# Kernel tuning notes

Measured on AMD Instinct MI355X. Metric: run time of the kernel, lower is better.

Reference implementation:

```python
import jax, jax.numpy as jnp
import numpy as np

B, T, L, V, E, H = 128, 64, 2, 32000, 768, 768
G = 4 * H  # gate dim
EPS = 1e-5


def setup_inputs() -> dict:
    key = jax.random.key(0)
    ks = jax.random.split(key, 12)
    s = 1.0 / np.sqrt(H)
    message = jax.random.randint(ks[0], (B, T), 0, V, dtype=jnp.int64)
    message_lengths = jax.random.randint(ks[1], (B,), 1, T + 1, dtype=jnp.int64)
    return {
        "message": message,
        "message_lengths": message_lengths,
        "embedding_table": jax.random.normal(ks[2], (V, E), jnp.float32),
        "W_ih": jax.random.uniform(ks[3], (L, G, E), jnp.float32, -s, s),
        "W_hh": jax.random.uniform(ks[4], (L, G, H), jnp.float32, -s, s),
        "b_ih": jax.random.uniform(ks[5], (L, G), jnp.float32, -s, s),
        "b_hh": jax.random.uniform(ks[6], (L, G), jnp.float32, -s, s),
        "gamma_h": 1.0 + 0.1 * jax.random.normal(ks[7], (H,), jnp.float32),
        "beta_h": 0.1 * jax.random.normal(ks[8], (H,), jnp.float32),
        "gamma_c": 1.0 + 0.1 * jax.random.normal(ks[9], (H,), jnp.float32),
        "beta_c": 0.1 * jax.random.normal(ks[10], (H,), jnp.float32),
    }


def _layernorm(x, g, b):
    mu = jnp.mean(x, axis=-1, keepdims=True)
    var = jnp.mean(jnp.square(x - mu), axis=-1, keepdims=True)
    return (x - mu) * jax.lax.rsqrt(var + EPS) * g + b


def reference(message, message_lengths, embedding_table, W_ih, W_hh, b_ih, b_hh,
              gamma_h, beta_h, gamma_c, beta_c):
    emb = embedding_table[message]  # [B, T, E]
    # Precompute input projections for all steps/layers (every layer sees the
    # raw embedding at each step, matching the original code).
    x_proj = jnp.einsum('bte,lge->tblg', emb, W_ih) + b_ih  # [T, B, L, G]
    mask = jnp.ones((B, H), emb.dtype)  # dropout_rate=None -> ones mask

    h0 = jnp.zeros((L, B, H), emb.dtype)
    c0 = jnp.zeros((L, B, H), emb.dtype)

    def step(carry, x_t):  # x_t: [B, L, G]
        h, c = carry
        new_h, new_c = [], []
        h_last = None
        for l in range(L):
            gates = x_t[:, l] + h[l] @ W_hh[l].T + b_hh[l]  # [B, G]
            i_g, f_g, g_g, o_g = jnp.split(gates, 4, axis=-1)
            c_t = jax.nn.sigmoid(f_g) * c[l] + jax.nn.sigmoid(i_g) * jnp.tanh(g_g)
            h_t = jax.nn.sigmoid(o_g) * jnp.tanh(c_t)
            h_t = _layernorm(h_t * mask, gamma_h, beta_h)
            c_t = _layernorm(c_t, gamma_c, beta_c)
            new_h.append(h_t)
            new_c.append(c_t)
            h_last = h_t
        return (jnp.stack(new_h), jnp.stack(new_c)), h_last

    _, hidden_all = jax.lax.scan(step, (h0, c0), x_proj)  # [T, B, H]
    hidden_all = hidden_all.transpose(1, 0, 2)  # [B, T, H]
    idx = (message_lengths - 1)[:, None, None]  # [B, 1, 1]
    encoded = jnp.take_along_axis(hidden_all, idx, axis=1)[:, 0]  # [B, H]
    return encoded
```

## Files before the change

### kernel.cpp

```cpp
#include <hip/hip_runtime.h>
#include <stdint.h>

#define T_LEN 64
#define B_SZ  128
#define H_SZ  768
#define G_SZ  3072
#define E_SZ  768
#define LN_EPS 1e-5f

typedef __bf16 bf16x8 __attribute__((ext_vector_type(8)));
typedef float  f32x4  __attribute__((ext_vector_type(4)));
typedef short  short8 __attribute__((ext_vector_type(8)));

__device__ __forceinline__ float bf2f(unsigned short h) {
  unsigned int u = ((unsigned int)h) << 16;
  return __builtin_bit_cast(float, u);
}
__device__ __forceinline__ unsigned short f2bf(float f) {
  unsigned int u = __builtin_bit_cast(unsigned int, f);
  u += 0x7fffu + ((u >> 16) & 1u);
  return (unsigned short)(u >> 16);
}
__device__ __forceinline__ void split8(float4 v0, float4 v1, short8& hi, short8& lo) {
  float v[8] = {v0.x, v0.y, v0.z, v0.w, v1.x, v1.y, v1.z, v1.w};
#pragma unroll
  for (int j = 0; j < 8; ++j) {
    unsigned short h = f2bf(v[j]);
    hi[j] = (short)h;
    lo[j] = (short)f2bf(v[j] - bf2f(h));
  }
}
__device__ __forceinline__ void st_wt(void* p, unsigned long long v) {
  __hip_atomic_store((unsigned long long*)p, v, __ATOMIC_RELAXED,
                     __HIP_MEMORY_SCOPE_AGENT);
}

__global__ void prep_kernel(const int* __restrict__ msg,
                            const float* __restrict__ table,
                            const float* __restrict__ W_ih,
                            const float* __restrict__ W_hh,
                            const float* __restrict__ b_ih,
                            const float* __restrict__ b_hh,
                            const float* __restrict__ gamma_h,
                            const float* __restrict__ beta_h,
                            unsigned short* __restrict__ A_hi,
                            unsigned short* __restrict__ A_lo,
                            unsigned short* __restrict__ Wih_hi,
                            unsigned short* __restrict__ Wih_lo,
                            unsigned short* __restrict__ Whh_hi,
                            unsigned short* __restrict__ Whh_lo,
                            float* __restrict__ SWp,
                            float* __restrict__ Sbeta,
                            float* __restrict__ bias,
                            unsigned int* __restrict__ bar) {
  int idx = blockIdx.x * blockDim.x + threadIdx.x;
  int stride = gridDim.x * blockDim.x;
  for (int c = idx; c < 8192 * 96; c += stride) {
    int n = c / 96;
    int ko = (c - n * 96) * 8;
    int b = n & 127, t = n >> 7;
    int m = msg[b * T_LEN + t];
    const float4* s4 = (const float4*)(table + (size_t)m * E_SZ + ko);
    short8 hi, lo;
    split8(s4[0], s4[1], hi, lo);
    *(short8*)(A_hi + (size_t)n * E_SZ + ko) = hi;
    *(short8*)(A_lo + (size_t)n * E_SZ + ko) = lo;
  }
  for (int c = idx; c < G_SZ * E_SZ / 8; c += stride) {
    int o8 = c * 8;
    {
      const float4* s4 = (const float4*)(W_ih + (size_t)G_SZ * E_SZ + o8);
      short8 hi, lo;
      split8(s4[0], s4[1], hi, lo);
      *(short8*)(Wih_hi + o8) = hi;
      *(short8*)(Wih_lo + o8) = lo;
    }
    {
      int g = o8 / H_SZ;
      int j = o8 - g * H_SZ;
      const float4* s4 = (const float4*)(W_hh + (size_t)G_SZ * H_SZ + o8);
      const float4* g4 = (const float4*)(gamma_h + j);
      float4 v0 = s4[0], v1 = s4[1];
      float4 w0 = g4[0], w1 = g4[1];
      v0.x *= w0.x; v0.y *= w0.y; v0.z *= w0.z; v0.w *= w0.w;
      v1.x *= w1.x; v1.y *= w1.y; v1.z *= w1.z; v1.w *= w1.w;
      short8 hi, lo;
      split8(v0, v1, hi, lo);
      *(short8*)(Whh_hi + o8) = hi;
      *(short8*)(Whh_lo + o8) = lo;
    }
  }
  for (int g = idx; g < G_SZ; g += stride) {
    const float4* wr = (const float4*)(W_hh + (size_t)G_SZ * H_SZ + (size_t)g * H_SZ);
    const float4* gm = (const float4*)gamma_h;
    const float4* bt = (const float4*)beta_h;
    float sw = 0.f, sb = 0.f;
    for (int i = 0; i < H_SZ / 4; ++i) {
      float4 wv = wr[i], gv = gm[i], bv = bt[i];
      sw += wv.x * gv.x + wv.y * gv.y + wv.z * gv.z + wv.w * gv.w;
      sb += wv.x * bv.x + wv.y * bv.y + wv.z * bv.z + wv.w * bv.w;
    }
    SWp[g] = sw;
    Sbeta[g] = sb;
    bias[g] = b_ih[G_SZ + g] + b_hh[G_SZ + g];
  }
  for (int c = idx; c < 18432; c += stride) bar[c] = 0u;
}

#define K2_STR 56

__global__ __launch_bounds__(256) void xproj_kernel(
    const unsigned short* __restrict__ A_hi, const unsigned short* __restrict__ A_lo,
    const unsigned short* __restrict__ B_hi, const unsigned short* __restrict__ B_lo,
    const float* __restrict__ bias, void* __restrict__ Xout, int x_is_f32) {
  __shared__ float smemf[7168];
  unsigned short* AsH = (unsigned short*)smemf;
  unsigned short* AsL = AsH + 64 * K2_STR;
  unsigned short* BsH = AsL + 64 * K2_STR;
  unsigned short* BsL = BsH + 64 * K2_STR;

  int bid = blockIdx.x;
  int mchunk = bid / 384;
  int r = bid - mchunk * 384;
  int nb = r >> 3;
  int mb = (mchunk << 3) + (r & 7);
  int m0 = mb * 64, n0 = nb * 64;
  int tid = threadIdx.x;
  int w = tid >> 6, lane = tid & 63;
  int wm = w & 1, wn = w >> 1;
  int rs = tid >> 2, ks = (tid & 3) * 8;
  int lrow = lane & 15, lk = (lane >> 4) * 8;

  f32x4 acc[2][2] = {};
  const unsigned short* gA = A_hi + (size_t)(m0 + rs) * E_SZ + ks;
  const unsigned short* gAl = A_lo + (size_t)(m0 + rs) * E_SZ + ks;
  const unsigned short* gB = B_hi + (size_t)(n0 + rs) * E_SZ + ks;
  const unsigned short* gBl = B_lo + (size_t)(n0 + rs) * E_SZ + ks;
  short8 vah = *(const short8*)gA;
  short8 val = *(const short8*)gAl;
  short8 vbh = *(const short8*)gB;
  short8 vbl = *(const short8*)gBl;
  for (int kt = 0; kt < 24; ++kt) {
    __syncthreads();
    *(short8*)(AsH + rs * K2_STR + ks) = vah;
    *(short8*)(AsL + rs * K2_STR + ks) = val;
    *(short8*)(BsH + rs * K2_STR + ks) = vbh;
    *(short8*)(BsL + rs * K2_STR + ks) = vbl;
    __syncthreads();
    if (kt < 23) {
      int k0 = (kt + 1) * 32;
      vah = *(const short8*)(gA + k0);
      val = *(const short8*)(gAl + k0);
      vbh = *(const short8*)(gB + k0);
      vbl = *(const short8*)(gBl + k0);
    }
    bf16x8 ah0 = *(const bf16x8*)(AsH + (wm * 32 +      lrow) * K2_STR + lk);
    bf16x8 ah1 = *(const bf16x8*)(AsH + (wm * 32 + 16 + lrow) * K2_STR + lk);
    bf16x8 al0 = *(const bf16x8*)(AsL + (wm * 32 +      lrow) * K2_STR + lk);
    bf16x8 al1 = *(const bf16x8*)(AsL + (wm * 32 + 16 + lrow) * K2_STR + lk);
    bf16x8 bh0 = *(const bf16x8*)(BsH + (wn * 32 +      lrow) * K2_STR + lk);
    bf16x8 bh1 = *(const bf16x8*)(BsH + (wn * 32 + 16 + lrow) * K2_STR + lk);
    bf16x8 bl0 = *(const bf16x8*)(BsL + (wn * 32 +      lrow) * K2_STR + lk);
    bf16x8 bl1 = *(const bf16x8*)(BsL + (wn * 32 + 16 + lrow) * K2_STR + lk);
    acc[0][0] = __builtin_amdgcn_mfma_f32_16x16x32_bf16(ah0, bh0, acc[0][0], 0, 0, 0);
    acc[1][0] = __builtin_amdgcn_mfma_f32_16x16x32_bf16(ah1, bh0, acc[1][0], 0, 0, 0);
    acc[0][1] = __builtin_amdgcn_mfma_f32_16x16x32_bf16(ah0, bh1, acc[0][1], 0, 0, 0);
    acc[1][1] = __builtin_amdgcn_mfma_f32_16x16x32_bf16(ah1, bh1, acc[1][1], 0, 0, 0);
    acc[0][0] = __builtin_amdgcn_mfma_f32_16x16x32_bf16(al0, bh0, acc[0][0], 0, 0, 0);
    acc[1][0] = __builtin_amdgcn_mfma_f32_16x16x32_bf16(al1, bh0, acc[1][0], 0, 0, 0);
    acc[0][1] = __builtin_amdgcn_mfma_f32_16x16x32_bf16(al0, bh1, acc[0][1], 0, 0, 0);
    acc[1][1] = __builtin_amdgcn_mfma_f32_16x16x32_bf16(al1, bh1, acc[1][1], 0, 0, 0);
    acc[0][0] = __builtin_amdgcn_mfma_f32_16x16x32_bf16(ah0, bl0, acc[0][0], 0, 0, 0);
    acc[1][0] = __builtin_amdgcn_mfma_f32_16x16x32_bf16(ah1, bl0, acc[1][0], 0, 0, 0);
    acc[0][1] = __builtin_amdgcn_mfma_f32_16x16x32_bf16(ah0, bl1, acc[0][1], 0, 0, 0);
    acc[1][1] = __builtin_amdgcn_mfma_f32_16x16x32_bf16(ah1, bl1, acc[1][1], 0, 0, 0);
  }
  __syncthreads();
  float* Cs = smemf;
  int quad = lane >> 4;
#pragma unroll
  for (int mt = 0; mt < 2; ++mt)
#pragma unroll
    for (int nt = 0; nt < 2; ++nt) {
      int mloc = wm * 32 + mt * 16 + quad * 4;
      int nloc = wn * 32 + nt * 16 + lrow;
#pragma unroll
      for (int rr = 0; rr < 4; ++rr) Cs[nloc * 72 + mloc + rr] = acc[mt][nt][rr];
    }
  __syncthreads();
  int t = mb >> 1, bbase = (mb & 1) * 64;
#pragma unroll
  for (int rep = 0; rep < 2; ++rep) {
    int n = (tid >> 3) + rep * 32;
    int c = (tid & 7) * 8;
    float bv = bias[n0 + n];
    float v[8];
#pragma unroll
    for (int j = 0; j < 8; ++j) v[j] = Cs[n * 72 + c + j] + bv;
    size_t off = ((size_t)t * G_SZ + (n0 + n)) * B_SZ + bbase + c;
    if (x_is_f32) {
      float4* dst = (float4*)((float*)Xout + off);
      dst[0] = make_float4(v[0], v[1], v[2], v[3]);
      dst[1] = make_float4(v[4], v[5], v[6], v[7]);
    } else {
      short8 o;
#pragma unroll
      for (int j = 0; j < 8; ++j) o[j] = (short)f2bf(v[j]);
      *(short8*)((unsigned short*)Xout + off) = o;
    }
  }
}

__device__ __forceinline__ void gridbar(unsigned int* leaf, unsigned int* root,
                                        int idx, int sub) {
  __syncthreads();
  if (threadIdx.x == 0) {
    asm volatile("" ::: "memory");
    unsigned int old = __hip_atomic_fetch_add(&leaf[idx * 128 + sub * 16], 1u,
                                              __ATOMIC_RELAXED, __HIP_MEMORY_SCOPE_AGENT);
    if (old == 11u)
      __hip_atomic_fetch_add(&root[idx * 16], 1u,
                             __ATOMIC_RELAXED, __HIP_MEMORY_SCOPE_AGENT);
    while (__hip_atomic_load(&root[idx * 16], __ATOMIC_RELAXED,
                             __HIP_MEMORY_SCOPE_AGENT) < 8u)
      __builtin_amdgcn_s_sleep(2);
    asm volatile("" ::: "memory");
  }
  __syncthreads();
}

extern __shared__ char lstm_smem[];

__global__ __launch_bounds__(128) void lstm_kernel(
    const unsigned short* __restrict__ Whh_lo,
    const unsigned short* __restrict__ Whh_hi,
    const void* __restrict__ X, int x_is_f32,
    const float* __restrict__ SWp, const float* __restrict__ Sbeta,
    const float* __restrict__ gamma_h, const float* __restrict__ beta_h,
    const float* __restrict__ gamma_c, const float* __restrict__ beta_c,
    const int* __restrict__ lens,
    unsigned short* __restrict__ Hbuf, float* __restrict__ part,
    unsigned int* __restrict__ bar, float* __restrict__ out) {
  unsigned short* WtH = (unsigned short*)lstm_smem;
  unsigned short* WtL = WtH + 32 * 776;
  float* glds   = (float*)(WtL + 32 * 776);
  float* pstat2 = glds + 2304;
  float* rstat4 = pstat2 + 512;
  float* rstat  = rstat4 + 256;
  float* ghs = rstat + 256;
  float* bhs = ghs + 8;
  float* gcs = bhs + 8;
  float* bcs = gcs + 8;

  int bidx = blockIdx.x;
  int jb = bidx % 96, rb = bidx / 96;
  int j0 = jb * 8, b0 = rb * 64;
  int tid = threadIdx.x;
  int w = tid >> 6, lane = tid & 63;
  int lrow = lane & 15, lkq = lane >> 4;
  int sub = jb / 12;
  unsigned int* leaf = bar;
  unsigned int* root = bar + 16384;

  for (int c = tid; c < 3072; c += 128) {
    int row = c / 96, ko = (c - row * 96) * 8;
    size_t goff = ((size_t)((row >> 3) * H_SZ + j0 + (row & 7))) * H_SZ + ko;
    *(short8*)(&WtH[row * 776 + ko]) = *(const short8*)(Whh_hi + goff);
    *(short8*)(&WtL[row * 776 + ko]) = *(const short8*)(Whh_lo + goff);
  }
  if (tid < 8) {
    ghs[tid] = gamma_h[j0 + tid]; bhs[tid] = beta_h[j0 + tid];
    gcs[tid] = gamma_c[j0 + tid]; bcs[tid] = beta_c[j0 + tid];
  }

  int row = tid & 63;
  int half = tid >> 6;
  int jjq = half * 4;
  int mylen = lens[b0 + row];
  int bb = w * 32;
  int gate4_[2], jjl_[2];
  float mySW_[2], mySb_[2];
  const unsigned short* wbH[2];
  const unsigned short* wbL[2];
  size_t gglob[2];
#pragma unroll
  for (int gg = 0; gg < 2; ++gg) {
    int grow = gg * 16 + lrow;
    gate4_[gg] = grow >> 3; jjl_[gg] = grow & 7;
    gglob[gg] = (size_t)gate4_[gg] * H_SZ + j0 + jjl_[gg];
    mySW_[gg] = SWp[gglob[gg]];
    mySb_[gg] = Sbeta[gglob[gg]];
    wbH[gg] = &WtH[(size_t)grow * 776];
    wbL[gg] = &WtL[(size_t)grow * 776];
  }
  float c4[4], h4[4];
  float xv[2][2][4];
  __syncthreads();

  {
#pragma unroll
    for (int gg = 0; gg < 2; ++gg) {
      size_t xbase = ((size_t)0 * G_SZ + gglob[gg]) * B_SZ + b0 + bb + lkq * 4;
#pragma unroll
      for (int mt = 0; mt < 2; ++mt) {
        float xr[4];
        if (x_is_f32) {
          float4 p = *(const float4*)((const float*)X + xbase + mt * 16);
          xr[0] = p.x; xr[1] = p.y; xr[2] = p.z; xr[3] = p.w;
        } else {
          ushort4 p = *(const ushort4*)((const unsigned short*)X + xbase + mt * 16);
          xr[0] = bf2f(p.x); xr[1] = bf2f(p.y); xr[2] = bf2f(p.z); xr[3] = bf2f(p.w);
        }
#pragma unroll
        for (int rr = 0; rr < 4; ++rr)
          glds[(gate4_[gg] * 8 + jjl_[gg]) * 72 + bb + mt * 16 + lkq * 4 + rr] = xr[rr];
      }
    }
  }
  __syncthreads();
  {
    float ph = 0.f, ph2 = 0.f, pc = 0.f, pc2 = 0.f;
#pragma unroll
    for (int q = 0; q < 4; ++q) {
      int jj = jjq + q;
      float iv = glds[(0 * 8 + jj) * 72 + row];
      float gv = glds[(2 * 8 + jj) * 72 + row];
      float ov = glds[(3 * 8 + jj) * 72 + row];
      float si = 1.f / (1.f + expf(-iv));
      float so = 1.f / (1.f + expf(-ov));
      float cn = si * tanhf(gv);
      float hp = so * tanhf(cn);
      c4[q] = cn; h4[q] = hp;
      ph += hp; ph2 += hp * hp; pc += cn; pc2 += cn * cn;
    }
    size_t hx = (((size_t)0 * 128 + b0 + row) * 96 + jb) * 16 + jjq;
    ushort4 hiv, lov;
    hiv.x = f2bf(h4[0]); hiv.y = f2bf(h4[1]); hiv.z = f2bf(h4[2]); hiv.w = f2bf(h4[3]);
    lov.x = f2bf(h4[0] - bf2f(hiv.x)); lov.y = f2bf(h4[1] - bf2f(hiv.y));
    lov.z = f2bf(h4[2] - bf2f(hiv.z)); lov.w = f2bf(h4[3] - bf2f(hiv.w));
    st_wt(&Hbuf[hx], __builtin_bit_cast(unsigned long long, hiv));
    st_wt(&Hbuf[hx + 8], __builtin_bit_cast(unsigned long long, lov));
    *(f32x4*)&pstat2[(row * 2 + half) * 4] = f32x4{ph, ph2, pc, pc2};
  }
  __syncthreads();
  {
    int f = tid * 2;
    float2 v;
    v.x = pstat2[(f >> 2) * 8 + (f & 3)] + pstat2[(f >> 2) * 8 + 4 + (f & 3)];
    v.y = pstat2[((f + 1) >> 2) * 8 + ((f + 1) & 3)] +
          pstat2[((f + 1) >> 2) * 8 + 4 + ((f + 1) & 3)];
    st_wt(&part[((size_t)(0 * 2 + rb) * 96 + jb) * 256 + f],
          __builtin_bit_cast(unsigned long long, v));
  }
  {
#pragma unroll
    for (int gg = 0; gg < 2; ++gg) {
      size_t xbase = ((size_t)1 * G_SZ + gglob[gg]) * B_SZ + b0 + bb + lkq * 4;
#pragma unroll
      for (int mt = 0; mt < 2; ++mt) {
        if (x_is_f32) {
          float4 p = *(const float4*)((const float*)X + xbase + mt * 16);
          xv[gg][mt][0] = p.x; xv[gg][mt][1] = p.y;
          xv[gg][mt][2] = p.z; xv[gg][mt][3] = p.w;
        } else {
          ushort4 p = *(const ushort4*)((const unsigned short*)X + xbase + mt * 16);
          xv[gg][mt][0] = bf2f(p.x); xv[gg][mt][1] = bf2f(p.y);
          xv[gg][mt][2] = bf2f(p.z); xv[gg][mt][3] = bf2f(p.w);
        }
      }
    }
  }
  gridbar(leaf, root, 0 * 2 + rb, sub);

  for (int t = 1; t < T_LEN; ++t) {
    f32x4 acc[2][2] = {};
    {
      const unsigned short* hb[2];
#pragma unroll
      for (int mt = 0; mt < 2; ++mt)
        hb[mt] = Hbuf + ((size_t)(t - 1) * 128 + b0 + bb + mt * 16 + lrow) * 1536;
#pragma unroll 8
      for (int kt = 0; kt < 24; ++kt) {
        int k0 = kt * 32 + lkq * 8;
        int co = (kt * 4 + lkq) * 16;
        bf16x8 wh0 = *(const bf16x8*)(wbH[0] + k0);
        bf16x8 wl0 = *(const bf16x8*)(wbL[0] + k0);
        bf16x8 wh1 = *(const bf16x8*)(wbH[1] + k0);
        bf16x8 wl1 = *(const bf16x8*)(wbL[1] + k0);
#pragma unroll
        for (int mt = 0; mt < 2; ++mt) {
          bf16x8 ah = *(const bf16x8*)(hb[mt] + co);
          bf16x8 al = *(const bf16x8*)(hb[mt] + co + 8);
          acc[mt][0] = __builtin_amdgcn_mfma_f32_16x16x32_bf16(ah, wh0, acc[mt][0], 0, 0, 0);
          acc[mt][0] = __builtin_amdgcn_mfma_f32_16x16x32_bf16(al, wh0, acc[mt][0], 0, 0, 0);
          acc[mt][0] = __builtin_amdgcn_mfma_f32_16x16x32_bf16(ah, wl0, acc[mt][0], 0, 0, 0);
          acc[mt][1] = __builtin_amdgcn_mfma_f32_16x16x32_bf16(ah, wh1, acc[mt][1], 0, 0, 0);
          acc[mt][1] = __builtin_amdgcn_mfma_f32_16x16x32_bf16(al, wh1, acc[mt][1], 0, 0, 0);
          acc[mt][1] = __builtin_amdgcn_mfma_f32_16x16x32_bf16(ah, wl1, acc[mt][1], 0, 0, 0);
        }
      }
    }
    float psum0 = 0.f, psum1 = 0.f;
    {
      const float* pb = part + ((size_t)((t - 1) * 2 + rb) * 96) * 256 + tid * 2;
#pragma unroll 24
      for (int j = 0; j < 96; ++j) {
        float2 v = *(const float2*)(pb + j * 256);
        psum0 += v.x; psum1 += v.y;
      }
    }
    {
      int f = tid * 2;
      rstat4[f] = psum0;
      rstat4[f + 1] = psum1;
    }
    __syncthreads();
    if (tid < 64) {
      f32x4 s = *(f32x4*)&rstat4[tid * 4];
      float muh = s[0] * (1.f / 768.f), muc = s[2] * (1.f / 768.f);
      float vh = s[1] * (1.f / 768.f) - muh * muh;
      float vc = s[3] * (1.f / 768.f) - muc * muc;
      float rh = rsqrtf(vh + LN_EPS), rc = rsqrtf(vc + LN_EPS);
      *(f32x4*)&rstat[tid * 4] = f32x4{rh, muh * rh, rc, muc * rc};
    }
    __syncthreads();
    if (mylen == t) {
      float2 rv = *(float2*)&rstat[row * 4];
#pragma unroll
      for (int q = 0; q < 4; ++q)
        out[(size_t)(b0 + row) * H_SZ + j0 + jjq + q] =
            (rv.x * h4[q] - rv.y) * ghs[jjq + q] + bhs[jjq + q];
    }
#pragma unroll
    for (int mt = 0; mt < 2; ++mt) {
#pragma unroll
      for (int rr = 0; rr < 4; ++rr) {
        int r2 = bb + mt * 16 + lkq * 4 + rr;
        float2 rv = *(float2*)&rstat[r2 * 4];
#pragma unroll
        for (int gg = 0; gg < 2; ++gg)
          glds[(gate4_[gg] * 8 + jjl_[gg]) * 72 + r2] =
              xv[gg][mt][rr] + rv.x * acc[mt][gg][rr] - rv.y * mySW_[gg] + mySb_[gg];
      }
    }
    __syncthreads();
    {
      f32x4 rv = *(f32x4*)&rstat[row * 4];
      float ph = 0.f, ph2 = 0.f, pc = 0.f, pc2 = 0.f;
#pragma unroll
      for (int q = 0; q < 4; ++q) {
        int jj = jjq + q;
        float cprev = (rv[2] * c4[q] - rv[3]) * gcs[jj] + bcs[jj];
        float iv = glds[(0 * 8 + jj) * 72 + row];
        float fv = glds[(1 * 8 + jj) * 72 + row];
        float gv = glds[(2 * 8 + jj) * 72 + row];
        float ov = glds[(3 * 8 + jj) * 72 + row];
        float si = 1.f / (1.f + expf(-iv));
        float sf = 1.f / (1.f + expf(-fv));
        float so = 1.f / (1.f + expf(-ov));
        float cn = sf * cprev + si * tanhf(gv);
        float hp = so * tanhf(cn);
        c4[q] = cn; h4[q] = hp;
        ph += hp; ph2 += hp * hp; pc += cn; pc2 += cn * cn;
      }
      size_t hx = (((size_t)t * 128 + b0 + row) * 96 + jb) * 16 + jjq;
      ushort4 hiv, lov;
      hiv.x = f2bf(h4[0]); hiv.y = f2bf(h4[1]); hiv.z = f2bf(h4[2]); hiv.w = f2bf(h4[3]);
      lov.x = f2bf(h4[0] - bf2f(hiv.x)); lov.y = f2bf(h4[1] - bf2f(hiv.y));
      lov.z = f2bf(h4[2] - bf2f(hiv.z)); lov.w = f2bf(h4[3] - bf2f(hiv.w));
      st_wt(&Hbuf[hx], __builtin_bit_cast(unsigned long long, hiv));
      st_wt(&Hbuf[hx + 8], __builtin_bit_cast(unsigned long long, lov));
      *(f32x4*)&pstat2[(row * 2 + half) * 4] = f32x4{ph, ph2, pc, pc2};
    }
    __syncthreads();
    {
      int f = tid * 2;
      float2 v;
      v.x = pstat2[(f >> 2) * 8 + (f & 3)] + pstat2[(f >> 2) * 8 + 4 + (f & 3)];
      v.y = pstat2[((f + 1) >> 2) * 8 + ((f + 1) & 3)] +
            pstat2[((f + 1) >> 2) * 8 + 4 + ((f + 1) & 3)];
      st_wt(&part[((size_t)(t * 2 + rb) * 96 + jb) * 256 + f],
            __builtin_bit_cast(unsigned long long, v));
    }
    if (t < T_LEN - 1) {
#pragma unroll
      for (int gg = 0; gg < 2; ++gg) {
        size_t xbase = ((size_t)(t + 1) * G_SZ + gglob[gg]) * B_SZ + b0 + bb + lkq * 4;
#pragma unroll
        for (int mt = 0; mt < 2; ++mt) {
          if (x_is_f32) {
            float4 p = *(const float4*)((const float*)X + xbase + mt * 16);
            xv[gg][mt][0] = p.x; xv[gg][mt][1] = p.y;
            xv[gg][mt][2] = p.z; xv[gg][mt][3] = p.w;
          } else {
            ushort4 p = *(const ushort4*)((const unsigned short*)X + xbase + mt * 16);
            xv[gg][mt][0] = bf2f(p.x); xv[gg][mt][1] = bf2f(p.y);
            xv[gg][mt][2] = bf2f(p.z); xv[gg][mt][3] = bf2f(p.w);
          }
        }
      }
    }
    gridbar(leaf, root, t * 2 + rb, sub);
  }

  {
    float psum0 = 0.f, psum1 = 0.f;
    const float* pb = part + ((size_t)(63 * 2 + rb) * 96) * 256 + tid * 2;
#pragma unroll 24
    for (int j = 0; j < 96; ++j) {
      float2 v = *(const float2*)(pb + j * 256);
      psum0 += v.x; psum1 += v.y;
    }
    rstat4[tid * 2] = psum0;
    rstat4[tid * 2 + 1] = psum1;
  }
  __syncthreads();
  if (tid < 64) {
    f32x4 s = *(f32x4*)&rstat4[tid * 4];
    float muh = s[0] * (1.f / 768.f);
    float vh = s[1] * (1.f / 768.f) - muh * muh;
    float rh = rsqrtf(vh + LN_EPS);
    rstat[tid * 4] = rh;
    rstat[tid * 4 + 1] = muh * rh;
  }
  __syncthreads();
  if (mylen == T_LEN) {
    float2 rv = *(float2*)&rstat[row * 4];
#pragma unroll
    for (int q = 0; q < 4; ++q)
      out[(size_t)(b0 + row) * H_SZ + j0 + jjq + q] =
          (rv.x * h4[q] - rv.y) * ghs[jjq + q] + bhs[jjq + q];
  }
}

#define LSTM_LDS_BYTES 112896

extern "C" void kernel_launch(void* const* d_in, const int* in_sizes, int n_in,
                              void* d_out, int out_size, void* d_ws, size_t ws_size,
                              hipStream_t stream) {
  const int*   msg     = (const int*)d_in[0];
  const int*   lens    = (const int*)d_in[1];
  const float* table   = (const float*)d_in[2];
  const float* W_ih    = (const float*)d_in[3];
  const float* W_hh    = (const float*)d_in[4];
  const float* b_ih    = (const float*)d_in[5];
  const float* b_hh    = (const float*)d_in[6];
  const float* gamma_h = (const float*)d_in[7];
  const float* beta_h  = (const float*)d_in[8];
  const float* gamma_c = (const float*)d_in[9];
  const float* beta_c  = (const float*)d_in[10];
  float* out = (float*)d_out;

  static int attr_done = 0;
  if (!attr_done) {
    hipFuncSetAttribute((const void*)lstm_kernel,
                        hipFuncAttributeMaxDynamicSharedMemorySize,
                        LSTM_LDS_BYTES);
    attr_done = 1;
  }

  size_t szA = (size_t)8192 * 768 * 2;
  size_t szW = (size_t)3072 * 768 * 2;
  size_t szF = 3072 * 4;
  size_t szH = (size_t)T_LEN * 128 * 96 * 16 * 2;
  size_t szBar = 18432 * 4;
  size_t rest = 2 * szA + 4 * szW + 3 * szF + szH + szBar;
  size_t xf32 = (size_t)64 * 3072 * 128 * 4;
  int x_is_f32 = (ws_size >= xf32 + rest) ? 1 : 0;

  char* p = (char*)d_ws;
  void* X = (void*)p;               p += x_is_f32 ? xf32 : (xf32 / 2);
  unsigned short* A_hi   = (unsigned short*)p; p += szA;
  unsigned short* A_lo   = (unsigned short*)p; p += szA;
  unsigned short* Wih_hi = (unsigned short*)p; p += szW;
  unsigned short* Wih_lo = (unsigned short*)p; p += szW;
  unsigned short* Whh_hi = (unsigned short*)p; p += szW;
  unsigned short* Whh_lo = (unsigned short*)p; p += szW;
  float* SWp   = (float*)p;         p += szF;
  float* Sbeta = (float*)p;         p += szF;
  float* bias  = (float*)p;         p += szF;
  unsigned short* Hbuf = (unsigned short*)p; p += szH;
  unsigned int* bar = (unsigned int*)p;      p += szBar;
  float* part = (float*)A_hi;

  hipLaunchKernelGGL(prep_kernel, dim3(1024), dim3(256), 0, stream,
                     msg, table, W_ih, W_hh, b_ih, b_hh, gamma_h, beta_h,
                     A_hi, A_lo, Wih_hi, Wih_lo, Whh_hi, Whh_lo,
                     SWp, Sbeta, bias, bar);
  hipLaunchKernelGGL(xproj_kernel, dim3(6144), dim3(256), 0, stream,
                     A_hi, A_lo, Wih_hi, Wih_lo, bias, X, x_is_f32);

  void* kargs[] = { (void*)&Whh_lo, (void*)&Whh_hi, (void*)&X, (void*)&x_is_f32,
                    (void*)&SWp, (void*)&Sbeta,
                    (void*)&gamma_h, (void*)&beta_h, (void*)&gamma_c, (void*)&beta_c,
                    (void*)&lens, (void*)&Hbuf, (void*)&part,
                    (void*)&bar, (void*)&out };
  hipLaunchCooperativeKernel((void*)lstm_kernel, dim3(192), dim3(128), kargs,
                             LSTM_LDS_BYTES, stream);
}
```

Measured before the change: 1.572 ms.

## Overlap next-step X prefetch and partial-sum reduction with recurrent MFMA loop

Moves the load of next-step input projections to the start of each timestep so its latency hides behind the recurrent matmul. Interleaves the cross-block LayerNorm partial-sum reads into the MFMA k-loop instead of a separate serial loop after it. Replaces the LDS staging of statistics and one __syncthreads with a lane shuffle that pairs the h and c sums. This shortens the serial critical path between grid barriers, at the cost of extra registers held live across the MFMA loop.

Result: slower. 1.623 ms (+3.2%).

```diff
diff --git a/kernel.cpp b/kernel.cpp
--- a/kernel.cpp
+++ b/kernel.cpp
@@ -373,8 +373,29 @@
   gridbar(leaf, root, 0 * 2 + rb, sub);
 
   for (int t = 1; t < T_LEN; ++t) {
+    float xv2[2][2][4];
+    if (t < T_LEN - 1) {
+#pragma unroll
+      for (int gg = 0; gg < 2; ++gg) {
+        size_t xbase = ((size_t)(t + 1) * G_SZ + gglob[gg]) * B_SZ + b0 + bb + lkq * 4;
+#pragma unroll
+        for (int mt = 0; mt < 2; ++mt) {
+          if (x_is_f32) {
+            float4 p = *(const float4*)((const float*)X + xbase + mt * 16);
+            xv2[gg][mt][0] = p.x; xv2[gg][mt][1] = p.y;
+            xv2[gg][mt][2] = p.z; xv2[gg][mt][3] = p.w;
+          } else {
+            ushort4 p = *(const ushort4*)((const unsigned short*)X + xbase + mt * 16);
+            xv2[gg][mt][0] = bf2f(p.x); xv2[gg][mt][1] = bf2f(p.y);
+            xv2[gg][mt][2] = bf2f(p.z); xv2[gg][mt][3] = bf2f(p.w);
+          }
+        }
+      }
+    }
     f32x4 acc[2][2] = {};
+    float psum0 = 0.f, psum1 = 0.f;
     {
+      const float* pb = part + ((size_t)((t - 1) * 2 + rb) * 96) * 256 + tid * 2;
       const unsigned short* hb[2];
 #pragma unroll
       for (int mt = 0; mt < 2; ++mt)
@@ -398,30 +419,23 @@
           acc[mt][1] = __builtin_amdgcn_mfma_f32_16x16x32_bf16(al, wh1, acc[mt][1], 0, 0, 0);
           acc[mt][1] = __builtin_amdgcn_mfma_f32_16x16x32_bf16(ah, wl1, acc[mt][1], 0, 0, 0);
         }
+#pragma unroll
+        for (int j2 = 0; j2 < 4; ++j2) {
+          float2 v = *(const float2*)(pb + (kt * 4 + j2) * 256);
+          psum0 += v.x; psum1 += v.y;
+        }
       }
     }
-    float psum0 = 0.f, psum1 = 0.f;
     {
-      const float* pb = part + ((size_t)((t - 1) * 2 + rb) * 96) * 256 + tid * 2;
-#pragma unroll 24
-      for (int j = 0; j < 96; ++j) {
-        float2 v = *(const float2*)(pb + j * 256);
-        psum0 += v.x; psum1 += v.y;
+      float o0 = __shfl_xor(psum0, 1);
+      float o1 = __shfl_xor(psum1, 1);
+      if ((tid & 1) == 0) {
+        float muh = psum0 * (1.f / 768.f), muc = o0 * (1.f / 768.f);
+        float vh = psum1 * (1.f / 768.f) - muh * muh;
+        float vc = o1 * (1.f / 768.f) - muc * muc;
+        float rh = rsqrtf(vh + LN_EPS), rc = rsqrtf(vc + LN_EPS);
+        *(f32x4*)&rstat[(tid >> 1) * 4] = f32x4{rh, muh * rh, rc, muc * rc};
       }
-    }
-    {
-      int f = tid * 2;
-      rstat4[f] = psum0;
-      rstat4[f + 1] = psum1;
-    }
-    __syncthreads();
-    if (tid < 64) {
-      f32x4 s = *(f32x4*)&rstat4[tid * 4];
-      float muh = s[0] * (1.f / 768.f), muc = s[2] * (1.f / 768.f);
-      float vh = s[1] * (1.f / 768.f) - muh * muh;
-      float vc = s[3] * (1.f / 768.f) - muc * muc;
-      float rh = rsqrtf(vh + LN_EPS), rc = rsqrtf(vc + LN_EPS);
-      *(f32x4*)&rstat[tid * 4] = f32x4{rh, muh * rh, rc, muc * rc};
     }
     __syncthreads();
     if (mylen == t) {
@@ -484,21 +498,11 @@
     }
     if (t < T_LEN - 1) {
 #pragma unroll
-      for (int gg = 0; gg < 2; ++gg) {
-        size_t xbase = ((size_t)(t + 1) * G_SZ + gglob[gg]) * B_SZ + b0 + bb + lkq * 4;
-#pragma unroll
-        for (int mt = 0; mt < 2; ++mt) {
-          if (x_is_f32) {
-            float4 p = *(const float4*)((const float*)X + xbase + mt * 16);
-            xv[gg][mt][0] = p.x; xv[gg][mt][1] = p.y;
-            xv[gg][mt][2] = p.z; xv[gg][mt][3] = p.w;
-          } else {
-            ushort4 p = *(const ushort4*)((const unsigned short*)X + xbase + mt * 16);
-            xv[gg][mt][0] = bf2f(p.x); xv[gg][mt][1] = bf2f(p.y);
-            xv[gg][mt][2] = bf2f(p.z); xv[gg][mt][3] = bf2f(p.w);
-          }
-        }
-      }
+      for (int gg = 0; gg < 2; ++gg)
+#pragma unroll
+        for (int mt = 0; mt < 2; ++mt)
+#pragma unroll
+          for (int rr = 0; rr < 4; ++rr) xv[gg][mt][rr] = xv2[gg][mt][rr];
     }
     gridbar(leaf, root, t * 2 + rb, sub);
   }
```

## Add per-subgroup release flags to grid barrier and vectorize LN partial reduction

Applied to the files above, without the earlier changes.

The grid barrier now has the last arriving block write release flags into 8 separate cache lines, one per subgroup. Waiters poll their own subgroup flag instead of all polling a single root counter, which spreads the spin traffic. The LayerNorm partial-sum reduction also changes so each thread reads float4 values and the two thread halves split the 96 partials, combined in LDS. This adds barrier memory and a little more release latency on the critical path.

Result: faster. 1.490 ms (-5.2%).

```diff
diff --git a/kernel.cpp b/kernel.cpp
--- a/kernel.cpp
+++ b/kernel.cpp
@@ -33,6 +33,9 @@
 __device__ __forceinline__ void st_wt(void* p, unsigned long long v) {
   __hip_atomic_store((unsigned long long*)p, v, __ATOMIC_RELAXED,
                      __HIP_MEMORY_SCOPE_AGENT);
+}
+__device__ __forceinline__ void st_wt32(unsigned int* p, unsigned int v) {
+  __hip_atomic_store(p, v, __ATOMIC_RELAXED, __HIP_MEMORY_SCOPE_AGENT);
 }
 
 __global__ void prep_kernel(const int* __restrict__ msg,
@@ -104,7 +107,7 @@
     Sbeta[g] = sb;
     bias[g] = b_ih[G_SZ + g] + b_hh[G_SZ + g];
   }
-  for (int c = idx; c < 18432; c += stride) bar[c] = 0u;
+  for (int c = idx; c < 34816; c += stride) bar[c] = 0u;
 }
 
 #define K2_STR 56
@@ -212,18 +215,27 @@
 }
 
 __device__ __forceinline__ void gridbar(unsigned int* leaf, unsigned int* root,
-                                        int idx, int sub) {
+                                        unsigned int* rel, int idx, int sub) {
   __syncthreads();
   if (threadIdx.x == 0) {
     asm volatile("" ::: "memory");
+    bool released = false;
     unsigned int old = __hip_atomic_fetch_add(&leaf[idx * 128 + sub * 16], 1u,
                                               __ATOMIC_RELAXED, __HIP_MEMORY_SCOPE_AGENT);
-    if (old == 11u)
-      __hip_atomic_fetch_add(&root[idx * 16], 1u,
-                             __ATOMIC_RELAXED, __HIP_MEMORY_SCOPE_AGENT);
-    while (__hip_atomic_load(&root[idx * 16], __ATOMIC_RELAXED,
-                             __HIP_MEMORY_SCOPE_AGENT) < 8u)
-      __builtin_amdgcn_s_sleep(2);
+    if (old == 11u) {
+      unsigned int rold = __hip_atomic_fetch_add(&root[idx * 16], 1u,
+                                                 __ATOMIC_RELAXED, __HIP_MEMORY_SCOPE_AGENT);
+      if (rold == 7u) {
+#pragma unroll
+        for (int s = 0; s < 8; ++s) st_wt32(&rel[idx * 128 + s * 16], 1u);
+        released = true;
+      }
+    }
+    if (!released) {
+      while (__hip_atomic_load(&rel[idx * 128 + sub * 16], __ATOMIC_RELAXED,
+                               __HIP_MEMORY_SCOPE_AGENT) == 0u)
+        __builtin_amdgcn_s_sleep(2);
+    }
     asm volatile("" ::: "memory");
   }
   __syncthreads();
@@ -261,6 +273,7 @@
   int sub = jb / 12;
   unsigned int* leaf = bar;
   unsigned int* root = bar + 16384;
+  unsigned int* rel  = bar + 18432;
 
   for (int c = tid; c < 3072; c += 128) {
     int row = c / 96, ko = (c - row * 96) * 8;
@@ -370,7 +383,7 @@
       }
     }
   }
-  gridbar(leaf, root, 0 * 2 + rb, sub);
+  gridbar(leaf, root, rel, 0 * 2 + rb, sub);
 
   for (int t = 1; t < T_LEN; ++t) {
     f32x4 acc[2][2] = {};
@@ -400,23 +413,20 @@
         }
       }
     }
-    float psum0 = 0.f, psum1 = 0.f;
     {
-      const float* pb = part + ((size_t)((t - 1) * 2 + rb) * 96) * 256 + tid * 2;
-#pragma unroll 24
-      for (int j = 0; j < 96; ++j) {
-        float2 v = *(const float2*)(pb + j * 256);
-        psum0 += v.x; psum1 += v.y;
-      }
-    }
-    {
-      int f = tid * 2;
-      rstat4[f] = psum0;
-      rstat4[f + 1] = psum1;
+      const float* pb = part + ((size_t)((t - 1) * 2 + rb) * 96) * 256 + (tid & 63) * 4;
+      int p = tid >> 6;
+      f32x4 s = {};
+#pragma unroll 12
+      for (int j = 0; j < 48; ++j)
+        s += *(const f32x4*)(pb + (size_t)(2 * j + p) * 256);
+      *(f32x4*)&pstat2[((tid & 63) * 2 + p) * 4] = s;
     }
     __syncthreads();
     if (tid < 64) {
-      f32x4 s = *(f32x4*)&rstat4[tid * 4];
+      f32x4 a = *(f32x4*)&pstat2[(tid * 2) * 4];
+      f32x4 b = *(f32x4*)&pstat2[(tid * 2 + 1) * 4];
+      f32x4 s = a + b;
       float muh = s[0] * (1.f / 768.f), muc = s[2] * (1.f / 768.f);
       float vh = s[1] * (1.f / 768.f) - muh * muh;
       float vc = s[3] * (1.f / 768.f) - muc * muc;
@@ -500,7 +510,7 @@
         }
       }
     }
-    gridbar(leaf, root, t * 2 + rb, sub);
+    gridbar(leaf, root, rel, t * 2 + rb, sub);
   }
 
   {
@@ -563,7 +573,7 @@
   size_t szW = (size_t)3072 * 768 * 2;
   size_t szF = 3072 * 4;
   size_t szH = (size_t)T_LEN * 128 * 96 * 16 * 2;
-  size_t szBar = 18432 * 4;
+  size_t szBar = 34816 * 4;
   size_t rest = 2 * szA + 4 * szW + 3 * szF + szH + szBar;
   size_t xf32 = (size_t)64 * 3072 * 128 * 4;
   int x_is_f32 = (ws_size >= xf32 + rest) ? 1 : 0;
```
